# Performance work log

Hardware: AMD Instinct MI355X
Metric: run time of the kernel (lower is better)

Reference implementation:

```python
import jax, jax.numpy as jnp
import numpy as np

PAD = 0
V, D = 50000, 300
MUS = np.array([-0.9, -0.7, -0.5, -0.3, -0.1, 0.1, 0.3, 0.5, 0.7, 0.9, 1.0], dtype=np.float32)
SIGMAS = np.array([0.1] * 10 + [0.001], dtype=np.float32)


def setup_inputs() -> dict:
    key = jax.random.key(0)
    k1, k2, k3, k4, k5, k6, k7 = jax.random.split(key, 7)
    B, Q, T = 256, 16, 1024
    return {
        "posdoc": jax.random.randint(k1, (B, T), 0, V),
        "negdoc": jax.random.randint(k2, (B, T), 0, V),
        "query": jax.random.randint(k3, (B, Q), 0, V),
        "query_idf": jax.random.normal(k4, (B, Q), dtype=jnp.float32),
        "emb": jax.random.normal(k5, (V, D), dtype=jnp.float32) * 0.1,
        "mus": jnp.asarray(MUS),
        "sigmas": jnp.asarray(SIGMAS),
        "W": jax.random.normal(k6, (11, 1), dtype=jnp.float32) * 0.3,
        "b": jax.random.normal(k7, (1,), dtype=jnp.float32) * 0.01,
    }


def _get_score(doc_tok, query_tok, emb, mus, sigmas, W, b):
    q = emb[query_tok]                                    # [B,Q,D]
    d = emb[doc_tok]                                      # [B,T,D]
    qn = q / (jnp.linalg.norm(q, axis=-1, keepdims=True) + 1e-9)
    dn = d / (jnp.linalg.norm(d, axis=-1, keepdims=True) + 1e-9)
    sim = jnp.einsum('bqd,btd->bqt', qn, dn)              # cosine simmat [B,Q,T]
    pair_mask = (query_tok != PAD)[:, :, None] & (doc_tok != PAD)[:, None, :]
    sim = sim * pair_mask                                 # zero out pad pairs
    # RBF kernel bank: [B,K,Q,T]
    diff = sim[:, None, :, :] - mus[None, :, None, None]
    k = jnp.exp(-0.5 * diff * diff / (sigmas[None, :, None, None] ** 2))
    doc_k = jnp.sum(k, axis=3)                            # [B,K,Q]
    qmask = jnp.sum(sim, axis=2) != 0.0                   # [B,Q]
    log_k = jnp.where(qmask[:, None, :], jnp.log(doc_k + 1e-6), 0.0)
    query_k = jnp.sum(log_k, axis=2)                      # [B,K]
    return (query_k @ W + b)[:, 0]                        # [B]


def reference(posdoc, negdoc, query, query_idf, emb, mus, sigmas, W, b):
    pos = _get_score(posdoc, query, emb, mus, sigmas, W, b)
    neg = _get_score(negdoc, query, emb, mus, sigmas, W, b)
    return jnp.stack([pos, neg], axis=1)                  # [B,2]
```

## Files before the change

kernel.cpp:

```cpp
#include <hip/hip_runtime.h>
#include <math.h>

#define BQ 16
#define TT 1024
#define DD 300
#define KK 11
#define ND4 75
#define KPAD 320
#define NCH 4


typedef unsigned short u16;
typedef unsigned char u8;
typedef long long i64;
typedef float f32x4 __attribute__((ext_vector_type(4)));
typedef long long i64x2 __attribute__((ext_vector_type(2)));

__device__ __forceinline__ unsigned f2e4m3(float f) {
    unsigned u = __float_as_uint(f);
    unsigned s = (u >> 24) & 0x80u;
    float a = fabsf(f);
    unsigned code;
    if (a < 0.015625f) {
        code = (unsigned)(int)rintf(a * 512.0f);
    } else {
        unsigned au = u & 0x7fffffffu;
        au += 0x7ffffu + ((au >> 20) & 1u);
        int e32 = (int)(au >> 23) - 127;
        code = ((unsigned)(e32 + 7) << 3) | ((au >> 20) & 7u);
    }
    return s | code;
}

__device__ __forceinline__ int perm_dword(int j) {
    int g4   = j >> 4;
    int quad = (j >> 1) & 3;
    int odd  = (j >> 3) & 1;
    int lo   = j & 1;
    return (g4 << 4) | (quad << 2) | (odd << 1) | lo;
}

template<int OFF>
__device__ __forceinline__ void gload16(i64x2& dst, const u8* p) {
    asm volatile("global_load_dwordx4 %0, %1, off offset:%2"
                 : "=v"(dst) : "v"(p), "i"(OFF));
}

#define ISSUE_TILE(B, P)                                                    \
    gload16<0>((B)[0], P);   gload16<64>((B)[1], P);  gload16<128>((B)[2], P); \
    gload16<192>((B)[3], P); gload16<256>((B)[4], P);

#define TILE_WAIT(NSTR, B)                                                  \
    asm volatile("s_waitcnt vmcnt(" NSTR ")"                                \
        : "+v"((B)[0]), "+v"((B)[1]), "+v"((B)[2]), "+v"((B)[3]), "+v"((B)[4]))

__global__ __launch_bounds__(256) void knrm_norm_table(
    const float* __restrict__ emb, u8* __restrict__ table, int V)
{
    const int w    = (blockIdx.x * 256 + threadIdx.x) >> 6;
    const int lane = threadIdx.x & 63;
    if (w >= V) return;

    const float4* __restrict__ src = (const float4*)(emb + (size_t)w * DD);
    float4 v = make_float4(0.f, 0.f, 0.f, 0.f);
    float4 v2 = v;
    if (lane < ND4) v = src[lane];
    if (lane < ND4 - 64) v2 = src[64 + lane];
    float ssq = v.x * v.x + v.y * v.y + v.z * v.z + v.w * v.w
              + v2.x * v2.x + v2.y * v2.y + v2.z * v2.z + v2.w * v2.w;
    #pragma unroll
    for (int off = 32; off; off >>= 1) ssq += __shfl_xor(ssq, off);
    const float inv = (w == 0) ? 0.f : 1.f / (sqrtf(ssq) + 1e-9f);

    unsigned* __restrict__ dst = (unsigned*)(table + (size_t)w * KPAD);
    unsigned p = f2e4m3(v.x * inv) | (f2e4m3(v.y * inv) << 8)
               | (f2e4m3(v.z * inv) << 16) | (f2e4m3(v.w * inv) << 24);
    dst[perm_dword(lane)] = (lane < ND4) ? p : 0u;
    if (lane < 16) {
        unsigned p2 = f2e4m3(v2.x * inv) | (f2e4m3(v2.y * inv) << 8)
                    | (f2e4m3(v2.z * inv) << 16) | (f2e4m3(v2.w * inv) << 24);
        dst[perm_dword(64 + lane)] = (lane < ND4 - 64) ? p2 : 0u;
    }
}

__global__ __launch_bounds__(256, 2) void knrm_mfma(
    const int* __restrict__ posdoc, const int* __restrict__ negdoc,
    const int* __restrict__ query,
    const u8* __restrict__ table,
    const float* __restrict__ mus, const float* __restrict__ sigmas,
    float* __restrict__ part)
{
    __shared__ float red[4][BQ][12];

    const int bid   = blockIdx.x;
    const int pair  = bid >> 2;
    const int chunk = bid & 3;
    const int bb    = pair >> 1;
    const int* __restrict__ doc = (pair & 1) ? negdoc : posdoc;
    const int tid  = threadIdx.x;
    const int lane = tid & 63;
    const int wave = tid >> 6;
    const int quad = lane >> 4;
    const int m    = lane & 15;

    const int tbase = bb * TT + chunk * 256 + wave * 64 + m;
    int toks[4];
    #pragma unroll
    for (int t = 0; t < 4; ++t) toks[t] = doc[tbase + t * 16];
    const int qtok = query[bb * BQ + m];
    const u8* ap  = table + (size_t)qtok    * KPAD + quad * 16;
    const u8* bp0 = table + (size_t)toks[0] * KPAD + quad * 16;
    const u8* bp1 = table + (size_t)toks[1] * KPAD + quad * 16;
    const u8* bp2 = table + (size_t)toks[2] * KPAD + quad * 16;
    const u8* bp3 = table + (size_t)toks[3] * KPAD + quad * 16;

    float muk[10], ck[10];
    #pragma unroll
    for (int k = 0; k < 10; ++k) {
        muk[k] = mus[k];
        float sg = sigmas[k];
        ck[k] = -0.72134752f / (sg * sg);
    }

    float vacc[12][4];
    #pragma unroll
    for (int v = 0; v < 12; ++v)
        #pragma unroll
        for (int r = 0; r < 4; ++r) vacc[v][r] = 0.f;

    asm volatile("s_waitcnt vmcnt(0)" ::: "memory");

    i64x2 afr[5], ba[5], bb_[5], bc[5], bd[5];
    ISSUE_TILE(afr, ap);
    ISSUE_TILE(ba,  bp0);
    ISSUE_TILE(bb_, bp1);
    ISSUE_TILE(bc,  bp2);
    ISSUE_TILE(bd,  bp3);

    #define COMPUTE_TILE(B)                                                        \
    {                                                                              \
        f32x4 acc = {0.f, 0.f, 0.f, 0.f};                                          \
        _Pragma("unroll")                                                          \
        for (int g = 0; g < 5; ++g) {                                              \
            acc = __builtin_amdgcn_mfma_f32_16x16x32_fp8_fp8(afr[g].x, (B)[g].x, acc, 0, 0, 0); \
            acc = __builtin_amdgcn_mfma_f32_16x16x32_fp8_fp8(afr[g].y, (B)[g].y, acc, 0, 0, 0); \
        }                                                                          \
        _Pragma("unroll")                                                          \
        for (int r = 0; r < 4; ++r) {                                              \
            float s = acc[r];                                                      \
            vacc[11][r] += s;                                                      \
            vacc[10][r] += (s > 0.9f ? 1.f : 0.f);                                 \
            _Pragma("unroll")                                                      \
            for (int k = 0; k < 10; ++k) {                                         \
                float d = s - muk[k];                                              \
                vacc[k][r] += __builtin_amdgcn_exp2f(ck[k] * d * d);               \
            }                                                                      \
        }                                                                          \
    }

    TILE_WAIT("20", afr);
    TILE_WAIT("15", ba);
    COMPUTE_TILE(ba);
    TILE_WAIT("10", bb_);
    COMPUTE_TILE(bb_);
    TILE_WAIT("5", bc);
    COMPUTE_TILE(bc);
    TILE_WAIT("0", bd);
    COMPUTE_TILE(bd);
    #undef COMPUTE_TILE

    #pragma unroll
    for (int r = 0; r < 4; ++r) {
        #pragma unroll
        for (int off = 8; off; off >>= 1)
            #pragma unroll
            for (int v = 0; v < 12; ++v)
                vacc[v][r] += __shfl_down(vacc[v][r], off, 16);
        if (m == 0) {
            int q = quad * 4 + r;
            #pragma unroll
            for (int v = 0; v < 12; ++v) red[wave][q][v] = vacc[v][r];
        }
    }
    __syncthreads();

    if (tid < 192) {
        int v = tid >> 4, q = tid & 15;
        float sum = red[0][q][v] + red[1][q][v] + red[2][q][v] + red[3][q][v];
        part[((size_t)bid * 12 + v) * BQ + q] = sum;
    }
}

__global__ __launch_bounds__(256) void knrm_partial(
    const int* __restrict__ posdoc, const int* __restrict__ negdoc,
    const int* __restrict__ query,
    const float* __restrict__ emb,
    const float* __restrict__ mus, const float* __restrict__ sigmas,
    float* __restrict__ ws)
{
    __shared__ __align__(16) float qs[BQ * DD];
    __shared__ float qscale[BQ];

    const int bid   = blockIdx.x;
    const int pair  = bid >> 2;
    const int chunk = bid & 3;
    const int bb    = pair >> 1;
    const int sel   = pair & 1;
    const int* __restrict__ doc = sel ? negdoc : posdoc;
    const int tid  = threadIdx.x;
    const int lane = tid & 63;
    const int wave = tid >> 6;

    float4* qs4 = (float4*)qs;
    for (int idx = tid; idx < BQ * ND4; idx += 256) {
        int q   = idx / ND4;
        int c   = idx - q * ND4;
        int tok = query[bb * BQ + q];
        qs4[idx] = ((const float4*)(emb + (size_t)tok * DD))[c];
    }
    __syncthreads();
    {
        int q = tid >> 4, sub = tid & 15;
        float ssq = 0.f;
        for (int i = sub; i < DD; i += 16) { float v = qs[q * DD + i]; ssq += v * v; }
        #pragma unroll
        for (int off = 8; off; off >>= 1) ssq += __shfl_down(ssq, off, 16);
        if (sub == 0) {
            int tok = query[bb * BQ + q];
            qscale[q] = (tok == 0) ? 0.f : 1.f / (sqrtf(ssq) + 1e-9f);
        }
    }
    __syncthreads();
    for (int idx = tid; idx < BQ * ND4; idx += 256) {
        int q = idx / ND4;
        float sc = qscale[q];
        float4 v = qs4[idx];
        v.x *= sc; v.y *= sc; v.z *= sc; v.w *= sc;
        qs4[idx] = v;
    }
    __syncthreads();

    const int tok = doc[bb * TT + chunk * 256 + tid];
    const float4* __restrict__ rowp = (const float4*)(emb + (size_t)tok * DD);
    float acc[BQ];
    #pragma unroll
    for (int q = 0; q < BQ; ++q) acc[q] = 0.f;
    float dss = 0.f;
    #pragma unroll 5
    for (int d4 = 0; d4 < ND4; ++d4) {
        float4 dv = rowp[d4];
        dss += dv.x * dv.x + dv.y * dv.y + dv.z * dv.z + dv.w * dv.w;
        #pragma unroll
        for (int q = 0; q < BQ; ++q) {
            float4 qv = qs4[q * ND4 + d4];
            acc[q] += dv.x * qv.x + dv.y * qv.y + dv.z * qv.z + dv.w * qv.w;
        }
    }
    const float invd = (tok == 0) ? 0.f : 1.f / (sqrtf(dss) + 1e-9f);

    float muk[KK], ck[KK];
    #pragma unroll
    for (int k = 0; k < KK; ++k) {
        muk[k] = mus[k];
        float sg = sigmas[k];
        ck[k] = -0.72134752f / (sg * sg);
    }
    __syncthreads();
    float* red = qs;
    const int grp = wave * 4 + (lane >> 4);
    const bool wr = (lane & 15) == 0;
    for (int q = 0; q < BQ; ++q) {
        float s = acc[q] * invd;
        float vals[12];
        vals[11] = s;
        #pragma unroll
        for (int k = 0; k < KK; ++k) {
            float d = s - muk[k];
            vals[k] = __builtin_amdgcn_exp2f(ck[k] * d * d);
        }
        #pragma unroll
        for (int off = 8; off; off >>= 1)
            #pragma unroll
            for (int v = 0; v < 12; ++v)
                vals[v] += __shfl_down(vals[v], off, 16);
        if (wr) {
            #pragma unroll
            for (int v = 0; v < 12; ++v) red[(grp * BQ + q) * 12 + v] = vals[v];
        }
    }
    __syncthreads();
    if (tid < 192) {
        int v = tid >> 4, q = tid & 15;
        float sum = 0.f;
        #pragma unroll
        for (int g = 0; g < 16; ++g) sum += red[(g * BQ + q) * 12 + v];
        ws[((size_t)(pair * 4 + chunk) * 12 + v) * BQ + q] = sum;
    }
}

__global__ __launch_bounds__(192) void knrm_final(
    const float* __restrict__ part,
    const float* __restrict__ Wv, const float* __restrict__ bv,
    float* __restrict__ out, int nchunk)
{
    __shared__ float dock[12 * BQ];
    __shared__ float lsum[KK];
    const int pair = blockIdx.x;
    const int tid  = threadIdx.x;
    {
        int v = tid >> 4, q = tid & 15;
        float sum = 0.f;
        for (int c = 0; c < nchunk; ++c)
            sum += part[((size_t)(pair * nchunk + c) * 12 + v) * BQ + q];
        dock[v * BQ + q] = sum;
    }
    __syncthreads();
    if (tid < 176) {
        int k = tid >> 4, q = tid & 15;
        float qm = dock[11 * BQ + q];
        float lv = (qm != 0.0f) ? logf(dock[k * BQ + q] + 1e-6f) : 0.f;
        #pragma unroll
        for (int off = 8; off; off >>= 1) lv += __shfl_down(lv, off, 16);
        if (q == 0) lsum[k] = lv;
    }
    __syncthreads();
    if (tid == 0) {
        float sc = bv[0];
        #pragma unroll
        for (int k = 0; k < KK; ++k) sc += lsum[k] * Wv[k];
        out[pair] = sc;
    }
}

extern "C" void kernel_launch(void* const* d_in, const int* in_sizes, int n_in,
                              void* d_out, int out_size, void* d_ws, size_t ws_size,
                              hipStream_t stream) {
    const int*   posdoc = (const int*)  d_in[0];
    const int*   negdoc = (const int*)  d_in[1];
    const int*   query  = (const int*)  d_in[2];
    const float* emb    = (const float*)d_in[4];
    const float* mus    = (const float*)d_in[5];
    const float* sigmas = (const float*)d_in[6];
    const float* Wv     = (const float*)d_in[7];
    const float* bv     = (const float*)d_in[8];
    float* out = (float*)d_out;

    const int V = in_sizes[4] / DD;
    const size_t table_bytes = (size_t)V * KPAD;
    const size_t part_bytes  = (size_t)512 * NCH * 12 * BQ * sizeof(float);

    if (ws_size >= table_bytes + part_bytes) {
        u8*    table = (u8*)d_ws;
        float* part  = (float*)((char*)d_ws + table_bytes);
        knrm_norm_table<<<dim3((V + 3) / 4), dim3(256), 0, stream>>>(emb, table, V);
        knrm_mfma<<<dim3(512 * NCH), dim3(256), 0, stream>>>(
            posdoc, negdoc, query, table, mus, sigmas, part);
        knrm_final<<<dim3(512), dim3(192), 0, stream>>>(part, Wv, bv, out, NCH);
    } else {
        float* part = (float*)d_ws;
        knrm_partial<<<dim3(512 * 4), dim3(256), 0, stream>>>(
            posdoc, negdoc, query, emb, mus, sigmas, part);
        knrm_final<<<dim3(512), dim3(192), 0, stream>>>(part, Wv, bv, out, 4);
    }
}
```

Baseline: 145.3 us.

## Replace ten RBF exps with recurrence, double-buffer tiles, raise occupancy

```diff
diff --git a/kernel.cpp b/kernel.cpp
--- a/kernel.cpp
+++ b/kernel.cpp
@@ -83,7 +83,7 @@
     }
 }
 
-__global__ __launch_bounds__(256, 2) void knrm_mfma(
+__global__ __launch_bounds__(256, 3) void knrm_mfma(
     const int* __restrict__ posdoc, const int* __restrict__ negdoc,
     const int* __restrict__ query,
     const u8* __restrict__ table,
@@ -114,14 +114,6 @@
     const u8* bp2 = table + (size_t)toks[2] * KPAD + quad * 16;
     const u8* bp3 = table + (size_t)toks[3] * KPAD + quad * 16;
 
-    float muk[10], ck[10];
-    #pragma unroll
-    for (int k = 0; k < 10; ++k) {
-        muk[k] = mus[k];
-        float sg = sigmas[k];
-        ck[k] = -0.72134752f / (sg * sg);
-    }
-
     float vacc[12][4];
     #pragma unroll
     for (int v = 0; v < 12; ++v)
@@ -130,12 +122,13 @@
 
     asm volatile("s_waitcnt vmcnt(0)" ::: "memory");
 
-    i64x2 afr[5], ba[5], bb_[5], bc[5], bd[5];
+    i64x2 afr[5], b0[5], b1[5];
     ISSUE_TILE(afr, ap);
-    ISSUE_TILE(ba,  bp0);
-    ISSUE_TILE(bb_, bp1);
-    ISSUE_TILE(bc,  bp2);
-    ISSUE_TILE(bd,  bp3);
+    ISSUE_TILE(b0,  bp0);
+    ISSUE_TILE(b1,  bp1);
+
+    const float C4 = 0.018315639f, C8 = 3.3546263e-4f,
+                C12 = 6.1442124e-6f, C16 = 1.1253517e-7f;
 
     #define COMPUTE_TILE(B)                                                        \
     {                                                                              \
@@ -150,23 +143,37 @@
             float s = acc[r];                                                      \
             vacc[11][r] += s;                                                      \
             vacc[10][r] += (s > 0.9f ? 1.f : 0.f);                                 \
-            _Pragma("unroll")                                                      \
-            for (int k = 0; k < 10; ++k) {                                         \
-                float d = s - muk[k];                                              \
-                vacc[k][r] += __builtin_amdgcn_exp2f(ck[k] * d * d);               \
-            }                                                                      \
+            float sm = s - 0.1f;                                                   \
+            float E5 = __builtin_amdgcn_exp2f(-72.134752f * sm * sm);              \
+            float R  = __builtin_amdgcn_exp2f(28.853901f * s);                     \
+            float Ri = __builtin_amdgcn_rcpf(R);                                   \
+            float E6 = E5 * (R * C4);                                              \
+            float E7 = E6 * (R * C8);                                              \
+            float E8 = E7 * (R * C12);                                             \
+            float E9 = E8 * (R * C16);                                             \
+            float E4 = E5 * Ri;                                                    \
+            float E3 = E4 * (Ri * C4);                                             \
+            float E2 = E3 * (Ri * C8);                                             \
+            float E1 = E2 * (Ri * C12);                                            \
+            float E0 = E1 * (Ri * C16);                                            \
+            vacc[0][r] += E0; vacc[1][r] += E1; vacc[2][r] += E2;                  \
+            vacc[3][r] += E3; vacc[4][r] += E4; vacc[5][r] += E5;                  \
+            vacc[6][r] += E6; vacc[7][r] += E7; vacc[8][r] += E8;                  \
+            vacc[9][r] += E9;                                                      \
         }                                                                          \
     }
 
-    TILE_WAIT("20", afr);
-    TILE_WAIT("15", ba);
-    COMPUTE_TILE(ba);
-    TILE_WAIT("10", bb_);
-    COMPUTE_TILE(bb_);
-    TILE_WAIT("5", bc);
-    COMPUTE_TILE(bc);
-    TILE_WAIT("0", bd);
-    COMPUTE_TILE(bd);
+    TILE_WAIT("10", afr);
+    TILE_WAIT("5",  b0);
+    COMPUTE_TILE(b0);
+    ISSUE_TILE(b0, bp2);
+    TILE_WAIT("5",  b1);
+    COMPUTE_TILE(b1);
+    ISSUE_TILE(b1, bp3);
+    TILE_WAIT("5",  b0);
+    COMPUTE_TILE(b0);
+    TILE_WAIT("0",  b1);
+    COMPUTE_TILE(b1);
     #undef COMPUTE_TILE
 
     #pragma unroll
```

New measurement: 143.0 us. About the same (-1.6%).
